# Performance work log

Measured on AMD Instinct MI355X. Metric: run time of the kernel, lower is better.

Reference implementation:

```python
import jax, jax.numpy as jnp
import numpy as np

BATCH, N_FEATURES, D_MODEL = 8192, 8192, 1024


def setup_inputs() -> dict:
    key = jax.random.key(0)
    kx, kw = jax.random.split(key)
    # x: sparse feature activations in the original (COO); dense uniform here.
    x = jax.random.uniform(kx, (BATCH, N_FEATURES), dtype=jnp.float32)
    # Xavier-normal init for W_tr [n_features, d_model].
    std = float(np.sqrt(2.0 / (N_FEATURES + D_MODEL)))
    W_tr = jax.random.normal(kw, (N_FEATURES, D_MODEL), dtype=jnp.float32) * std
    bias = jnp.zeros((N_FEATURES,), dtype=jnp.float32)
    return {"x": x, "W_tr": W_tr, "bias": bias}


def reference(x, W_tr, bias):
    # h = x @ W_tr              : [B, n_features] @ [n_features, d_model] -> [B, d_model]
    # out = relu(h @ W_tr.T + b): [B, d_model] @ [d_model, n_features] -> [B, n_features]
    h = jnp.einsum("bf,fd->bd", x, W_tr)
    return jax.nn.relu(jnp.einsum("bd,fd->bf", h, W_tr) + bias)
```

## Files before the change

kernel.cpp:

```cpp
#include <hip/hip_runtime.h>
#include <hip/hip_bf16.h>
#include <stdint.h>

#define BATCH  8192
#define NFEAT  8192
#define DMODEL 1024

typedef unsigned short u16;
typedef __attribute__((ext_vector_type(8))) short  short8;
typedef __attribute__((ext_vector_type(4))) float  f32x4;

__device__ __forceinline__ u16 f2b(float f) {
    uint32_t u = __float_as_uint(f);
    u += 0x7fffu + ((u >> 16) & 1u);
    return (u16)(u >> 16);
}

__device__ __forceinline__ void gld16(const u16* g, void* l) {
    __builtin_amdgcn_global_load_lds(
        (const __attribute__((address_space(1))) void*)(uintptr_t)g,
        (__attribute__((address_space(3))) void*)(uint32_t)(uintptr_t)l,
        16, 0, 0);
}


__global__ void cvt_x_kernel(const float* __restrict__ x, u16* __restrict__ xb) {
    int i = blockIdx.x * blockDim.x + threadIdx.x;
    const float4* xv = (const float4*)x;
    float4 a = xv[2 * i];
    float4 b = xv[2 * i + 1];
    union { u16 u[8]; uint4 v; } o;
    o.u[0] = f2b(a.x); o.u[1] = f2b(a.y); o.u[2] = f2b(a.z); o.u[3] = f2b(a.w);
    o.u[4] = f2b(b.x); o.u[5] = f2b(b.y); o.u[6] = f2b(b.z); o.u[7] = f2b(b.w);
    ((uint4*)xb)[i] = o.v;
}

__global__ void cvt_w_kernel(const float* __restrict__ W,
                             u16* __restrict__ wb, u16* __restrict__ wt) {
    __shared__ u16 tile[64][65];
    const int f0 = blockIdx.x * 64;
    const int d0 = blockIdx.y * 64;
    const int t  = threadIdx.x;
#pragma unroll
    for (int rep = 0; rep < 16; ++rep) {
        int idx = rep * 256 + t;
        int r = idx >> 6, c = idx & 63;
        float v = W[(size_t)(f0 + r) * DMODEL + d0 + c];
        u16 u = f2b(v);
        tile[r][c] = u;
        wb[(size_t)(f0 + r) * DMODEL + d0 + c] = u;
    }
    __syncthreads();
#pragma unroll
    for (int rep = 0; rep < 16; ++rep) {
        int idx = rep * 256 + t;
        int r = idx >> 6, c = idx & 63;
        wt[(size_t)(d0 + r) * NFEAT + f0 + c] = tile[c][r];
    }
}

#define CBAR() do { asm volatile("" ::: "memory"); __builtin_amdgcn_s_barrier(); } while (0)


#define PREF(T, A0P, BP) do {                                                   \
        if ((T) < NT) {                                                         \
            const char* Abp = lds + ((T) % 3) * 32768 + wm * 16384 + l15 * 128; \
            const char* Bbp = lds + BOFF + ((T) & 1) * 16384 + wn * 4096 + l15 * 128; \
            _Pragma("unroll")                                                   \
            for (int fm = 0; fm < 4; ++fm) {                                    \
                A0P[fm][0] = *(const short8*)(Abp + fm * 2048 + ch0);           \
                A0P[fm][1] = *(const short8*)(Abp + fm * 2048 + (ch0 ^ 64));    \
            }                                                                   \
            _Pragma("unroll")                                                   \
            for (int nh = 0; nh < 2; ++nh) {                                    \
                BP[nh][0] = *(const short8*)(Bbp + nh * 2048 + ch0);            \
                BP[nh][1] = *(const short8*)(Bbp + nh * 2048 + (ch0 ^ 64));     \
            }                                                                   \
        }                                                                       \
    } while (0)

#define MMA0_(A0C, BC) do {                                                     \
        _Pragma("unroll")                                                       \
        for (int nh = 0; nh < 2; ++nh)                                          \
            _Pragma("unroll")                                                   \
            for (int ks = 0; ks < 2; ++ks)                                      \
                _Pragma("unroll")                                               \
                for (int fm = 0; fm < 4; ++fm)                                  \
                    acc[fm][nh] = __builtin_amdgcn_mfma_f32_16x16x32_bf16(      \
                        A0C[fm][ks], BC[nh][ks], acc[fm][nh], 0, 0, 0);         \
    } while (0)

#define MMA1_(BC) do {                                                          \
        _Pragma("unroll")                                                       \
        for (int nh = 0; nh < 2; ++nh)                                          \
            _Pragma("unroll")                                                   \
            for (int ks = 0; ks < 2; ++ks)                                      \
                _Pragma("unroll")                                               \
                for (int fm = 0; fm < 4; ++fm)                                  \
                    acc[4 + fm][nh] = __builtin_amdgcn_mfma_f32_16x16x32_bf16(  \
                        a1[fm][ks], BC[nh][ks], acc[4 + fm][nh], 0, 0, 0);      \
    } while (0)

#define GTILE(T, A0C, BC, A0P, BP) do {                                         \
        const char* Ab_ = lds + ((T) % 3) * 32768 + wm * 16384 + l15 * 128;     \
        _Pragma("unroll")                                                       \
        for (int fm = 0; fm < 4; ++fm) {                                        \
            a1[fm][0] = *(const short8*)(Ab_ + (4 + fm) * 2048 + ch0);          \
            a1[fm][1] = *(const short8*)(Ab_ + (4 + fm) * 2048 + (ch0 ^ 64));   \
        }                                                                       \
        STAGE_A((T) + 2);                                                       \
        __builtin_amdgcn_s_setprio(1);                                          \
        MMA0_(A0C, BC);                                                         \
        __builtin_amdgcn_s_setprio(0);                                          \
        STAGE_B((T) + 2);                                                       \
        if ((T) < NT - 2) asm volatile("s_waitcnt vmcnt(6)" ::: "memory");      \
        else              asm volatile("s_waitcnt vmcnt(0)" ::: "memory");      \
        CBAR();             \
        PREF((T) + 1, A0P, BP);                                                 \
        __builtin_amdgcn_s_setprio(1);                                          \
        MMA1_(BC);                                                              \
        __builtin_amdgcn_s_setprio(0);                                          \
    } while (0)

__global__ __launch_bounds__(512, 2)
void gemm1_pipe(const u16* __restrict__ A, const u16* __restrict__ B,
                u16* __restrict__ H, int N, int K) {
    const int NT = K >> 6;
    __shared__ __align__(1024) char lds[131072];
    const int BOFF = 98304;

    const int tid  = threadIdx.x;
    const int lane = tid & 63;
    const int wave = tid >> 6;
    const int wm   = wave >> 2;
    const int wn   = wave & 3;

    const int nwg = gridDim.x;
    const int swz = (blockIdx.x & 7) * (nwg >> 3) + (blockIdx.x >> 3);
    const int ntn = N >> 7;
    const int tm0 = (swz / ntn) << 8;
    const int tn0 = (swz % ntn) << 7;

    const int sr8 = lane >> 3;
    const int sg  = (lane & 7) ^ sr8;
    const int l15 = lane & 15, lhi = lane >> 4;
    const int ch0 = ((lhi ^ (lane & 7)) << 4);

    auto STAGE_A = [&](int tau) {
        if (tau < NT) {
            char* d = lds + (tau % 3) * 32768 + wave * 4096;
#pragma unroll
            for (int i = 0; i < 4; ++i)
                gld16(A + (size_t)(tm0 + wave * 32 + i * 8 + sr8) * K + ((size_t)tau << 6) + sg * 8,
                      d + i * 1024);
        }
    };
    auto STAGE_B = [&](int tau) {
        if (tau < NT) {
            char* d = lds + BOFF + (tau & 1) * 16384 + wave * 2048;
#pragma unroll
            for (int i = 0; i < 2; ++i)
                gld16(B + (size_t)(tn0 + wave * 16 + i * 8 + sr8) * K + ((size_t)tau << 6) + sg * 8,
                      d + i * 1024);
        }
    };

    short8 a0X[4][2], a0Y[4][2], a1[4][2];
    short8 bX[2][2], bY[2][2];
    f32x4  acc[8][2] = {};

    STAGE_A(0); STAGE_B(0);
    STAGE_A(1); STAGE_B(1);
    asm volatile("s_waitcnt vmcnt(6)" ::: "memory");
    __builtin_amdgcn_s_barrier();
    PREF(0, a0X, bX);

    for (int t = 0; t < NT; t += 2) {
        GTILE(t,     a0X, bX, a0Y, bY);
        GTILE(t + 1, a0Y, bY, a0X, bX);
    }
    __syncthreads();

    u16* lu = (u16*)lds;
#pragma unroll
    for (int fm = 0; fm < 8; ++fm)
#pragma unroll
        for (int nh = 0; nh < 2; ++nh) {
            const int col  = wn * 32 + nh * 16 + l15;
            const int row0 = wm * 128 + fm * 16 + lhi * 4;
#pragma unroll
            for (int r = 0; r < 4; ++r)
                lu[(row0 + r) * 128 + col] = f2b(acc[fm][nh][r]);
        }
    __syncthreads();
    const uint4* ls = (const uint4*)lds;
#pragma unroll
    for (int s = 0; s < 8; ++s) {
        int i = s * 512 + tid;
        int row = i >> 4;
        int col = (i & 15) * 8;
        *(uint4*)(H + (size_t)(tm0 + row) * N + (tn0 + col)) = ls[i];
    }
}

__global__ __launch_bounds__(512, 2)
void gemm2_pipe(const u16* __restrict__ A, const u16* __restrict__ B,
                float* __restrict__ O, const float* __restrict__ bias,
                int N, int K) {
    const int NT = 128;
    __shared__ __align__(1024) char lds[131072];
    const int BOFF = 98304;

    const int tid  = threadIdx.x;
    const int lane = tid & 63;
    const int wave = tid >> 6;
    const int wm   = wave >> 2;
    const int wn   = wave & 3;

    const int bid = blockIdx.x;
    const int cp  = ((bid & 7) << 3) | ((bid >> 3) & 7);
    const int mg  = bid >> 6;
    const int tn0     = cp << 7;
    const int tm_base = mg << 11;

    const int sr8 = lane >> 3;
    const int sg  = (lane & 7) ^ sr8;
    const int l15 = lane & 15, lhi = lane >> 4;
    const int ch0 = ((lhi ^ (lane & 7)) << 4);

    auto STAGE_A = [&](int tau) {
        if (tau < NT) {
            char* d = lds + (tau % 3) * 32768 + wave * 4096;
            const int rb = tm_base + ((tau >> 4) << 8) + wave * 32 + sr8;
            const size_t co = ((size_t)(tau & 15) << 6) + sg * 8;
#pragma unroll
            for (int i = 0; i < 4; ++i)
                gld16(A + (size_t)(rb + i * 8) * K + co, d + i * 1024);
        }
    };
    auto STAGE_B = [&](int tau) {
        if (tau < NT) {
            char* d = lds + BOFF + (tau & 1) * 16384 + wave * 2048;
            const size_t co = ((size_t)(tau & 15) << 6) + sg * 8;
#pragma unroll
            for (int i = 0; i < 2; ++i)
                gld16(B + (size_t)(tn0 + wave * 16 + i * 8 + sr8) * K + co, d + i * 1024);
        }
    };

    short8 a0X[4][2], a0Y[4][2], a1[4][2];
    short8 bX[2][2], bY[2][2];
    f32x4  acc[8][2] = {};

    const int ocol = tn0 + wn * 32;
    float bv[2];
#pragma unroll
    for (int nh = 0; nh < 2; ++nh) bv[nh] = bias[ocol + nh * 16 + l15];

    STAGE_A(0); STAGE_B(0);
    STAGE_A(1); STAGE_B(1);
    asm volatile("s_waitcnt vmcnt(6)" ::: "memory");
    __builtin_amdgcn_s_barrier();
    PREF(0, a0X, bX);

    for (int t = 0; t < NT; t += 2) {
        GTILE(t,     a0X, bX, a0Y, bY);
        GTILE(t + 1, a0Y, bY, a0X, bX);

        if (((t + 1) & 15) == 15) {
            const int seg  = (t + 1) >> 4;
            const int orow = tm_base + (seg << 8) + wm * 128;
#pragma unroll
            for (int fm = 0; fm < 8; ++fm) {
                const int row0 = orow + fm * 16 + lhi * 4;
#pragma unroll
                for (int nh = 0; nh < 2; ++nh) {
                    const int col = ocol + nh * 16 + l15;
#pragma unroll
                    for (int r = 0; r < 4; ++r) {
                        float v = acc[fm][nh][r] + bv[nh];
                        O[(size_t)(row0 + r) * N + col] = v > 0.f ? v : 0.f;
                        acc[fm][nh][r] = 0.f;
                    }
                }
            }
        }
    }
}

#undef GTILE
#undef PREF
#undef MMA0_
#undef MMA1_


extern "C" void kernel_launch(void* const* d_in, const int* in_sizes, int n_in,
                              void* d_out, int out_size, void* d_ws, size_t ws_size,
                              hipStream_t stream) {
    const float* x    = (const float*)d_in[0];
    const float* W    = (const float*)d_in[1];
    const float* bias = (const float*)d_in[2];
    float* out = (float*)d_out;

    char* ws = (char*)d_ws;
    u16* xb = (u16*)ws;
    u16* wt = (u16*)(ws + 134217728);
    u16* wb = (u16*)(ws + 134217728 + 16777216);
    u16* hb = (u16*)(ws + 134217728 + 2 * 16777216);

    cvt_x_kernel<<<(BATCH * NFEAT / 8) / 256, 256, 0, stream>>>(x, xb);
    cvt_w_kernel<<<dim3(NFEAT / 64, DMODEL / 64), 256, 0, stream>>>(W, wb, wt);

    gemm1_pipe<<<dim3((BATCH / 256) * (DMODEL / 128)), 512, 0, stream>>>(
        xb, wt, hb, DMODEL, NFEAT);

    gemm2_pipe<<<dim3(256), 512, 0, stream>>>(
        hb, wb, out, bias, NFEAT, DMODEL);
}
```

Measured before the change: 352.6 us.

## Interleave gemm2 segment epilogue stores with next segment's MMA tiles

The output epilogue of the second GEMM used to write the full 256-row segment after the last tile of that segment. It is now split into two halves. The first half is stored before the next segment's first tile, and the second half is issued between that tile's MMA0 and MMA1 phases, after the accumulators they use are freed. The vmcnt wait in those tiles is relaxed to 38 to account for the outstanding stores, so output writes overlap with matrix-core work. The segment loop is also restructured and unrolled, which risks higher code size and register pressure, and the hand-tuned vmcnt values must stay consistent.

```diff
diff --git a/kernel.cpp b/kernel.cpp
--- a/kernel.cpp
+++ b/kernel.cpp
@@ -101,7 +101,7 @@
                         a1[fm][ks], BC[nh][ks], acc[4 + fm][nh], 0, 0, 0);      \
     } while (0)
 
-#define GTILE(T, A0C, BC, A0P, BP) do {                                         \
+#define GTILEX(T, A0C, BC, A0P, BP, VM, EXTRA) do {                             \
         const char* Ab_ = lds + ((T) % 3) * 32768 + wm * 16384 + l15 * 128;     \
         _Pragma("unroll")                                                       \
         for (int fm = 0; fm < 4; ++fm) {                                        \
@@ -113,10 +113,11 @@
         MMA0_(A0C, BC);                                                         \
         __builtin_amdgcn_s_setprio(0);                                          \
         STAGE_B((T) + 2);                                                       \
-        if ((T) < NT - 2) asm volatile("s_waitcnt vmcnt(6)" ::: "memory");      \
+        if ((T) < NT - 2) asm volatile("s_waitcnt vmcnt(" #VM ")" ::: "memory");\
         else              asm volatile("s_waitcnt vmcnt(0)" ::: "memory");      \
         CBAR();             \
         PREF((T) + 1, A0P, BP);                                                 \
+        EXTRA;                                                                  \
         __builtin_amdgcn_s_setprio(1);                                          \
         MMA1_(BC);                                                              \
         __builtin_amdgcn_s_setprio(0);                                          \
@@ -176,8 +177,8 @@
     PREF(0, a0X, bX);
 
     for (int t = 0; t < NT; t += 2) {
-        GTILE(t,     a0X, bX, a0Y, bY);
-        GTILE(t + 1, a0Y, bY, a0X, bX);
+        GTILEX(t,     a0X, bX, a0Y, bY, 6, (void)0);
+        GTILEX(t + 1, a0Y, bY, a0X, bX, 6, (void)0);
     }
     __syncthreads();
 
@@ -257,38 +258,52 @@
 #pragma unroll
     for (int nh = 0; nh < 2; ++nh) bv[nh] = bias[ocol + nh * 16 + l15];
 
+#define STORE_HALF(SEGV, FM0) do {                                        \
+        const int orow_ = tm_base + ((SEGV) << 8) + wm * 128;             \
+        _Pragma("unroll")                                                 \
+        for (int fm = 0; fm < 4; ++fm) {                                  \
+            const int row0_ = orow_ + ((FM0) + fm) * 16 + lhi * 4;        \
+            _Pragma("unroll")                                             \
+            for (int nh = 0; nh < 2; ++nh) {                              \
+                const int col_ = ocol + nh * 16 + l15;                    \
+                _Pragma("unroll")                                         \
+                for (int r = 0; r < 4; ++r) {                             \
+                    float v = acc[(FM0) + fm][nh][r] + bv[nh];            \
+                    O[(size_t)(row0_ + r) * N + col_] = v > 0.f ? v : 0.f;\
+                    acc[(FM0) + fm][nh][r] = 0.f;                         \
+                }                                                         \
+            }                                                             \
+        }                                                                 \
+    } while (0)
+
     STAGE_A(0); STAGE_B(0);
     STAGE_A(1); STAGE_B(1);
     asm volatile("s_waitcnt vmcnt(6)" ::: "memory");
     __builtin_amdgcn_s_barrier();
     PREF(0, a0X, bX);
 
-    for (int t = 0; t < NT; t += 2) {
-        GTILE(t,     a0X, bX, a0Y, bY);
-        GTILE(t + 1, a0Y, bY, a0X, bX);
-
-        if (((t + 1) & 15) == 15) {
-            const int seg  = (t + 1) >> 4;
-            const int orow = tm_base + (seg << 8) + wm * 128;
-#pragma unroll
-            for (int fm = 0; fm < 8; ++fm) {
-                const int row0 = orow + fm * 16 + lhi * 4;
-#pragma unroll
-                for (int nh = 0; nh < 2; ++nh) {
-                    const int col = ocol + nh * 16 + l15;
-#pragma unroll
-                    for (int r = 0; r < 4; ++r) {
-                        float v = acc[fm][nh][r] + bv[nh];
-                        O[(size_t)(row0 + r) * N + col] = v > 0.f ? v : 0.f;
-                        acc[fm][nh][r] = 0.f;
-                    }
-                }
-            }
-        }
-    }
-}
-
-#undef GTILE
+    for (int seg = 0; seg < 8; ++seg) {
+        const int base = seg << 4;
+        if (seg == 0) {
+            GTILEX(0, a0X, bX, a0Y, bY, 6, (void)0);
+            GTILEX(1, a0Y, bY, a0X, bX, 6, (void)0);
+        } else {
+            STORE_HALF(seg - 1, 0);
+            GTILEX(base,     a0X, bX, a0Y, bY, 38, STORE_HALF(seg - 1, 4));
+            GTILEX(base + 1, a0Y, bY, a0X, bX, 38, (void)0);
+        }
+#pragma unroll
+        for (int tt = base + 2; tt < base + 16; tt += 2) {
+            GTILEX(tt,     a0X, bX, a0Y, bY, 6, (void)0);
+            GTILEX(tt + 1, a0Y, bY, a0X, bX, 6, (void)0);
+        }
+    }
+    STORE_HALF(7, 0);
+    STORE_HALF(7, 4);
+#undef STORE_HALF
+}
+
+#undef GTILEX
 #undef PREF
 #undef MMA0_
 #undef MMA1_
```

Measured after the change: 517.8 us. +46.8%, slower.

## Shrink gemm2 block to 128x128 tiles with 256 threads and 512 blocks

Applied to the files above, without the earlier changes.

Reworks the second GEMM so each block uses 4 waves covering a 128-row by 128-column output tile, in place of 8 waves over 256 rows. The grid doubles to 512 blocks and LDS use drops to 80 KB, which should allow more resident blocks per CU and better fill the 256 CUs. The cost is less reuse of each staged B tile per block, so B traffic from global memory and L2 roughly doubles, and the pipeline wait counts are retuned.

```diff
diff --git a/kernel.cpp b/kernel.cpp
--- a/kernel.cpp
+++ b/kernel.cpp
@@ -62,6 +62,28 @@
 #define CBAR() do { asm volatile("" ::: "memory"); __builtin_amdgcn_s_barrier(); } while (0)
 
 
+#define MMA0_(A0C, BC) do {                                                     \
+        _Pragma("unroll")                                                       \
+        for (int nh = 0; nh < 2; ++nh)                                          \
+            _Pragma("unroll")                                                   \
+            for (int ks = 0; ks < 2; ++ks)                                      \
+                _Pragma("unroll")                                               \
+                for (int fm = 0; fm < 4; ++fm)                                  \
+                    acc[fm][nh] = __builtin_amdgcn_mfma_f32_16x16x32_bf16(      \
+                        A0C[fm][ks], BC[nh][ks], acc[fm][nh], 0, 0, 0);         \
+    } while (0)
+
+#define MMA1_(BC) do {                                                          \
+        _Pragma("unroll")                                                       \
+        for (int nh = 0; nh < 2; ++nh)                                          \
+            _Pragma("unroll")                                                   \
+            for (int ks = 0; ks < 2; ++ks)                                      \
+                _Pragma("unroll")                                               \
+                for (int fm = 0; fm < 4; ++fm)                                  \
+                    acc[4 + fm][nh] = __builtin_amdgcn_mfma_f32_16x16x32_bf16(  \
+                        a1[fm][ks], BC[nh][ks], acc[4 + fm][nh], 0, 0, 0);      \
+    } while (0)
+
 #define PREF(T, A0P, BP) do {                                                   \
         if ((T) < NT) {                                                         \
             const char* Abp = lds + ((T) % 3) * 32768 + wm * 16384 + l15 * 128; \
@@ -77,28 +99,6 @@
                 BP[nh][1] = *(const short8*)(Bbp + nh * 2048 + (ch0 ^ 64));     \
             }                                                                   \
         }                                                                       \
-    } while (0)
-
-#define MMA0_(A0C, BC) do {                                                     \
-        _Pragma("unroll")                                                       \
-        for (int nh = 0; nh < 2; ++nh)                                          \
-            _Pragma("unroll")                                                   \
-            for (int ks = 0; ks < 2; ++ks)                                      \
-                _Pragma("unroll")                                               \
-                for (int fm = 0; fm < 4; ++fm)                                  \
-                    acc[fm][nh] = __builtin_amdgcn_mfma_f32_16x16x32_bf16(      \
-                        A0C[fm][ks], BC[nh][ks], acc[fm][nh], 0, 0, 0);         \
-    } while (0)
-
-#define MMA1_(BC) do {                                                          \
-        _Pragma("unroll")                                                       \
-        for (int nh = 0; nh < 2; ++nh)                                          \
-            _Pragma("unroll")                                                   \
-            for (int ks = 0; ks < 2; ++ks)                                      \
-                _Pragma("unroll")                                               \
-                for (int fm = 0; fm < 4; ++fm)                                  \
-                    acc[4 + fm][nh] = __builtin_amdgcn_mfma_f32_16x16x32_bf16(  \
-                        a1[fm][ks], BC[nh][ks], acc[4 + fm][nh], 0, 0, 0);      \
     } while (0)
 
 #define GTILE(T, A0C, BC, A0P, BP) do {                                         \
@@ -115,7 +115,7 @@
         STAGE_B((T) + 2);                                                       \
         if ((T) < NT - 2) asm volatile("s_waitcnt vmcnt(6)" ::: "memory");      \
         else              asm volatile("s_waitcnt vmcnt(0)" ::: "memory");      \
-        CBAR();             \
+        CBAR();                                                                 \
         PREF((T) + 1, A0P, BP);                                                 \
         __builtin_amdgcn_s_setprio(1);                                          \
         MMA1_(BC);                                                              \
@@ -203,25 +203,62 @@
     }
 }
 
-__global__ __launch_bounds__(512, 2)
-void gemm2_pipe(const u16* __restrict__ A, const u16* __restrict__ B,
-                float* __restrict__ O, const float* __restrict__ bias,
-                int N, int K) {
+#define PREF2(T, A0P, BP) do {                                                  \
+        if ((T) < NT) {                                                         \
+            const char* Abp = lds + ((T) % 3) * 16384 + l15 * 128;              \
+            const char* Bbp = lds + BOFF + ((T) & 1) * 16384 + wn * 4096 + l15 * 128; \
+            _Pragma("unroll")                                                   \
+            for (int fm = 0; fm < 4; ++fm) {                                    \
+                A0P[fm][0] = *(const short8*)(Abp + fm * 2048 + ch0);           \
+                A0P[fm][1] = *(const short8*)(Abp + fm * 2048 + (ch0 ^ 64));    \
+            }                                                                   \
+            _Pragma("unroll")                                                   \
+            for (int nh = 0; nh < 2; ++nh) {                                    \
+                BP[nh][0] = *(const short8*)(Bbp + nh * 2048 + ch0);            \
+                BP[nh][1] = *(const short8*)(Bbp + nh * 2048 + (ch0 ^ 64));     \
+            }                                                                   \
+        }                                                                       \
+    } while (0)
+
+#define GTILE2(T, A0C, BC, A0P, BP) do {                                        \
+        const char* Ab_ = lds + ((T) % 3) * 16384 + l15 * 128;                  \
+        _Pragma("unroll")                                                       \
+        for (int fm = 0; fm < 4; ++fm) {                                        \
+            a1[fm][0] = *(const short8*)(Ab_ + (4 + fm) * 2048 + ch0);          \
+            a1[fm][1] = *(const short8*)(Ab_ + (4 + fm) * 2048 + (ch0 ^ 64));   \
+        }                                                                       \
+        STAGE_A((T) + 2);                                                       \
+        __builtin_amdgcn_s_setprio(1);                                          \
+        MMA0_(A0C, BC);                                                         \
+        __builtin_amdgcn_s_setprio(0);                                          \
+        STAGE_B((T) + 2);                                                       \
+        if ((T) < NT - 2) asm volatile("s_waitcnt vmcnt(8)" ::: "memory");      \
+        else              asm volatile("s_waitcnt vmcnt(0)" ::: "memory");      \
+        CBAR();                                                                 \
+        PREF2((T) + 1, A0P, BP);                                                \
+        __builtin_amdgcn_s_setprio(1);                                          \
+        MMA1_(BC);                                                              \
+        __builtin_amdgcn_s_setprio(0);                                          \
+    } while (0)
+
+__global__ __launch_bounds__(256, 2)
+void gemm2_pipe2(const u16* __restrict__ A, const u16* __restrict__ B,
+                 float* __restrict__ O, const float* __restrict__ bias,
+                 int N, int K) {
     const int NT = 128;
-    __shared__ __align__(1024) char lds[131072];
-    const int BOFF = 98304;
+    __shared__ __align__(1024) char lds[81920];
+    const int BOFF = 49152;
 
     const int tid  = threadIdx.x;
     const int lane = tid & 63;
     const int wave = tid >> 6;
-    const int wm   = wave >> 2;
-    const int wn   = wave & 3;
+    const int wn   = wave;
 
     const int bid = blockIdx.x;
     const int cp  = ((bid & 7) << 3) | ((bid >> 3) & 7);
-    const int mg  = bid >> 6;
+    const int mg  = (bid >> 6) & 7;
     const int tn0     = cp << 7;
-    const int tm_base = mg << 11;
+    const int tm_base = mg << 10;
 
     const int sr8 = lane >> 3;
     const int sg  = (lane & 7) ^ sr8;
@@ -230,8 +267,8 @@
 
     auto STAGE_A = [&](int tau) {
         if (tau < NT) {
-            char* d = lds + (tau % 3) * 32768 + wave * 4096;
-            const int rb = tm_base + ((tau >> 4) << 8) + wave * 32 + sr8;
+            char* d = lds + (tau % 3) * 16384 + wave * 4096;
+            const int rb = tm_base + ((tau >> 4) << 7) + wave * 32 + sr8;
             const size_t co = ((size_t)(tau & 15) << 6) + sg * 8;
 #pragma unroll
             for (int i = 0; i < 4; ++i)
@@ -240,11 +277,12 @@
     };
     auto STAGE_B = [&](int tau) {
         if (tau < NT) {
-            char* d = lds + BOFF + (tau & 1) * 16384 + wave * 2048;
+            char* d = lds + BOFF + (tau & 1) * 16384 + wave * 4096;
+            const int rb = tn0 + wave * 32 + sr8;
             const size_t co = ((size_t)(tau & 15) << 6) + sg * 8;
 #pragma unroll
-            for (int i = 0; i < 2; ++i)
-                gld16(B + (size_t)(tn0 + wave * 16 + i * 8 + sr8) * K + co, d + i * 1024);
+            for (int i = 0; i < 4; ++i)
+                gld16(B + (size_t)(rb + i * 8) * K + co, d + i * 1024);
         }
     };
 
@@ -259,17 +297,16 @@
 
     STAGE_A(0); STAGE_B(0);
     STAGE_A(1); STAGE_B(1);
-    asm volatile("s_waitcnt vmcnt(6)" ::: "memory");
+    asm volatile("s_waitcnt vmcnt(8)" ::: "memory");
     __builtin_amdgcn_s_barrier();
-    PREF(0, a0X, bX);
+    PREF2(0, a0X, bX);
 
     for (int t = 0; t < NT; t += 2) {
-        GTILE(t,     a0X, bX, a0Y, bY);
-        GTILE(t + 1, a0Y, bY, a0X, bX);
+        GTILE2(t,     a0X, bX, a0Y, bY);
+        GTILE2(t + 1, a0Y, bY, a0X, bX);
 
         if (((t + 1) & 15) == 15) {
-            const int seg  = (t + 1) >> 4;
-            const int orow = tm_base + (seg << 8) + wm * 128;
+            const int orow = tm_base + (((t + 1) >> 4) << 7);
 #pragma unroll
             for (int fm = 0; fm < 8; ++fm) {
                 const int row0 = orow + fm * 16 + lhi * 4;
@@ -289,7 +326,9 @@
 }
 
 #undef GTILE
+#undef GTILE2
 #undef PREF
+#undef PREF2
 #undef MMA0_
 #undef MMA1_
 
@@ -314,6 +353,6 @@
     gemm1_pipe<<<dim3((BATCH / 256) * (DMODEL / 128)), 512, 0, stream>>>(
         xb, wt, hb, DMODEL, NFEAT);
 
-    gemm2_pipe<<<dim3(256), 512, 0, stream>>>(
+    gemm2_pipe2<<<dim3(512), 256, 0, stream>>>(
         hb, wb, out, bias, NFEAT, DMODEL);
 }
```

Measured after the change: 350.3 us. About the same (-0.6%).
